# Optimization experiments

Measured on AMD Instinct MI355X. Metric: run time of the kernel, lower is better.

## Reference

```python
import jax, jax.numpy as jnp
import numpy as np

N = 131072   # total atoms in flat batch
E = 262144   # total bonds (directed edges)
G = 4096     # number of molecules (graphs)
FN = 30      # atom feature dim
FE = 11      # bond feature dim
H = 256      # hidden_dim
L = 5        # num GINE layers
BN_EPS = 1e-5


def _bn(x, g, b, m, v):
    # BatchNorm1d in eval mode: affine with running stats
    return g * (x - m) * jax.lax.rsqrt(v + BN_EPS) + b


def setup_inputs() -> dict:
    key = jax.random.key(0)
    ks = jax.random.split(key, 48)
    s = 0.05  # weight scale to keep 5-layer residual stack well-conditioned
    inp = {
        'x': jax.random.normal(ks[0], (N, FN), jnp.float32),
        'edge_index': jax.random.randint(ks[1], (2, E), 0, N),
        'batch': jnp.sort(jax.random.randint(ks[2], (N,), 0, G)),
        'edge_attr': jax.random.normal(ks[3], (E, FE), jnp.float32),
        # encoders
        'enc_w': s * jax.random.normal(ks[4], (FN, H), jnp.float32),
        'enc_b': jnp.zeros((H,), jnp.float32),
        'bond_w': s * jax.random.normal(ks[5], (FE, H), jnp.float32),
        'bond_b': jnp.zeros((H,), jnp.float32),
        # per-layer GINE params (stacked over L)
        'eps': jnp.zeros((L,), jnp.float32),
        'w1': s * jax.random.normal(ks[6], (L, H, 2 * H), jnp.float32),
        'b1': jnp.zeros((L, 2 * H), jnp.float32),
        'ibn_g': 1.0 + 0.1 * jax.random.normal(ks[7], (L, 2 * H), jnp.float32),
        'ibn_b': 0.1 * jax.random.normal(ks[8], (L, 2 * H), jnp.float32),
        'ibn_m': 0.1 * jax.random.normal(ks[9], (L, 2 * H), jnp.float32),
        'ibn_v': jnp.ones((L, 2 * H), jnp.float32),
        'w2': s * jax.random.normal(ks[10], (L, 2 * H, H), jnp.float32),
        'b2': jnp.zeros((L, H), jnp.float32),
        'obn_g': 1.0 + 0.1 * jax.random.normal(ks[11], (L, H), jnp.float32),
        'obn_b': 0.1 * jax.random.normal(ks[12], (L, H), jnp.float32),
        'obn_m': 0.1 * jax.random.normal(ks[13], (L, H), jnp.float32),
        'obn_v': jnp.ones((L, H), jnp.float32),
        # classifier
        'cw1': s * jax.random.normal(ks[14], (2 * H, H), jnp.float32),
        'cb1': jnp.zeros((H,), jnp.float32),
        'c1g': 1.0 + 0.1 * jax.random.normal(ks[15], (H,), jnp.float32),
        'c1b': 0.1 * jax.random.normal(ks[16], (H,), jnp.float32),
        'c1m': 0.1 * jax.random.normal(ks[17], (H,), jnp.float32),
        'c1v': jnp.ones((H,), jnp.float32),
        'cw2': s * jax.random.normal(ks[18], (H, H // 2), jnp.float32),
        'cb2': jnp.zeros((H // 2,), jnp.float32),
        'c2g': 1.0 + 0.1 * jax.random.normal(ks[19], (H // 2,), jnp.float32),
        'c2b': 0.1 * jax.random.normal(ks[20], (H // 2,), jnp.float32),
        'c2m': 0.1 * jax.random.normal(ks[21], (H // 2,), jnp.float32),
        'c2v': jnp.ones((H // 2,), jnp.float32),
        'cw3': s * jax.random.normal(ks[22], (H // 2, 1), jnp.float32),
        'cb3': jnp.zeros((1,), jnp.float32),
    }
    return inp


def reference(x, edge_index, batch, edge_attr,
              enc_w, enc_b, bond_w, bond_b,
              eps, w1, b1, ibn_g, ibn_b, ibn_m, ibn_v,
              w2, b2, obn_g, obn_b, obn_m, obn_v,
              cw1, cb1, c1g, c1b, c1m, c1v,
              cw2, cb2, c2g, c2b, c2m, c2v,
              cw3, cb3):
    n = x.shape[0]
    src, dst = edge_index[0], edge_index[1]
    h = x @ enc_w + enc_b                      # [N, H]
    e = edge_attr @ bond_w + bond_b           # [E, H]
    for i in range(L):
        h_in = h
        # GINEConv: (1+eps)*x_i + sum_j relu(x_j + e_ji), then MLP
        msg = jax.nn.relu(h[src] + e)                          # [E, H] gather
        agg = jax.ops.segment_sum(msg, dst, num_segments=n)    # [N, H] scatter-add
        z = (1.0 + eps[i]) * h + agg
        z = jax.nn.relu(_bn(z @ w1[i] + b1[i], ibn_g[i], ibn_b[i], ibn_m[i], ibn_v[i]))
        z = z @ w2[i] + b2[i]
        # outer BN + relu (dropout is identity in eval) + residual
        h = jax.nn.relu(_bn(z, obn_g[i], obn_b[i], obn_m[i], obn_v[i])) + h_in
    # global mean + max pooling by graph id
    counts = jax.ops.segment_sum(jnp.ones((n,), h.dtype), batch, num_segments=G)
    sums = jax.ops.segment_sum(h, batch, num_segments=G)
    mean_p = sums / jnp.maximum(counts, 1.0)[:, None]
    max_p = jax.ops.segment_max(h, batch, num_segments=G)
    max_p = jnp.where(counts[:, None] > 0, max_p, 0.0)
    p = jnp.concatenate([mean_p, max_p], axis=1)               # [G, 2H]
    # classifier (eval mode: dropout off, BN uses running stats)
    q = jax.nn.relu(_bn(p @ cw1 + cb1, c1g, c1b, c1m, c1v))
    q = jax.nn.relu(_bn(q @ cw2 + cb2, c2g, c2b, c2m, c2v))
    out = q @ cw3 + cb3
    return out[:, 0]                                           # [G]
```

## Files before the change

kernel.cpp:

```cpp
#include <hip/hip_runtime.h>
#include <math.h>

#define NA 131072
#define NE 262144
#define NG 4096
#define FN 30
#define FE 11
#define H  256
#define H2 512
#define NL 5
#define BN_EPS 1e-5f
#define KP 32

typedef _Float16 f16x8 __attribute__((ext_vector_type(8)));
typedef _Float16 f16x4 __attribute__((ext_vector_type(4)));
typedef float f32x4 __attribute__((ext_vector_type(4)));

#define GLOAD16(GP, LP) \
    __builtin_amdgcn_global_load_lds((const __attribute__((address_space(1))) void*)(GP), \
                                     (__attribute__((address_space(3))) void*)(LP), 16, 0, 0)

static char* g_buf = nullptr;
__attribute__((constructor)) static void _alloc_private_ws() {
    void* p = nullptr;
    if (hipMalloc(&p, (size_t)320 * 1024 * 1024) == hipSuccess) g_buf = (char*)p;
}

__global__ __launch_bounds__(256) void prep_w_all(const float* __restrict__ w, int K, int N,
                                                  _Float16* __restrict__ hT) {
    const float* wl = w + (size_t)blockIdx.z * K * N;
    _Float16* hTl = hT + (size_t)blockIdx.z * K * N;
    __shared__ float t[32][33];
    const int k0 = blockIdx.x * 32, n0 = blockIdx.y * 32;
    const int tx = threadIdx.x & 31, ty = threadIdx.x >> 5;
    #pragma unroll
    for (int i = 0; i < 4; ++i)
        t[ty + i * 8][tx] = wl[(size_t)(k0 + ty + i * 8) * N + n0 + tx];
    __syncthreads();
    #pragma unroll
    for (int i = 0; i < 4; ++i)
        hTl[(size_t)(n0 + ty + i * 8) * K + k0 + tx] = (_Float16)t[tx][ty + i * 8];
}

__global__ __launch_bounds__(256) void prep_w1s(const float* __restrict__ w1,
                                                _Float16* __restrict__ o) {
    const float* wl = w1 + (size_t)blockIdx.z * H * H2;
    _Float16* ol = o + (size_t)blockIdx.z * H * H2;
    const int c = blockIdx.x * 256 + threadIdx.x;
    const int slot = c & 3, row = (c >> 2) & 255, hk = c >> 10;
    const int n = (hk >> 3) * 256 + row;
    const int kb = (hk & 7) * 32 + (slot ^ ((row >> 1) & 3)) * 8;
    f16x8 v;
    #pragma unroll
    for (int e = 0; e < 8; ++e) v[e] = (_Float16)wl[(size_t)(kb + e) * H2 + n];
    *(f16x8*)(ol + (size_t)c * 8) = v;
}

__global__ __launch_bounds__(256) void prep_w2s(const float* __restrict__ w2,
                                                _Float16* __restrict__ o) {
    const float* wl = w2 + (size_t)blockIdx.z * H2 * H;
    _Float16* ol = o + (size_t)blockIdx.z * H2 * H;
    const int c = blockIdx.x * 256 + threadIdx.x;
    const int slot = c & 3, row = (c >> 2) & 255, ks = c >> 10;
    const int kb = ks * 32 + (slot ^ ((row >> 1) & 3)) * 8;
    f16x8 v;
    #pragma unroll
    for (int e = 0; e < 8; ++e) v[e] = (_Float16)wl[(size_t)(kb + e) * H + row];
    *(f16x8*)(ol + (size_t)c * 8) = v;
}

__global__ __launch_bounds__(256) void prep_wpad(const float* __restrict__ w, int K_IN,
                                                 _Float16* __restrict__ wT) {
    const int n = threadIdx.x;
    #pragma unroll
    for (int kk = 0; kk < KP / 8; ++kk) {
        f16x8 v;
        #pragma unroll
        for (int j = 0; j < 8; ++j) {
            const int k = kk * 8 + j;
            v[j] = (k < K_IN) ? (_Float16)w[(size_t)k * H + n] : (_Float16)0.0f;
        }
        *(f16x8*)(wT + (size_t)n * KP + kk * 8) = v;
    }
}

__global__ __launch_bounds__(256) void prep_x16(const float* __restrict__ x,
                                                _Float16* __restrict__ x16) {
    const int row = blockIdx.x * 64 + (threadIdx.x >> 2);
    const int g = threadIdx.x & 3;
    f16x8 v;
    #pragma unroll
    for (int j = 0; j < 8; ++j) {
        const int c = g * 8 + j;
        v[j] = (c < FN) ? (_Float16)x[(size_t)row * FN + c] : (_Float16)0.0f;
    }
    *(f16x8*)(x16 + (size_t)row * KP + g * 8) = v;
}

__global__ __launch_bounds__(256) void prep_ea16(const float* __restrict__ eattr,
                                                 const int2* __restrict__ se,
                                                 _Float16* __restrict__ ea16) {
    const int t = blockIdx.x * 64 + (threadIdx.x >> 2);
    const int g = threadIdx.x & 3;
    const int e = se[t].y;
    f16x8 v;
    #pragma unroll
    for (int j = 0; j < 8; ++j) {
        const int c = g * 8 + j;
        v[j] = (c < FE) ? (_Float16)eattr[(size_t)e * FE + c] : (_Float16)0.0f;
    }
    *(f16x8*)(ea16 + (size_t)t * KP + g * 8) = v;
}

__global__ __launch_bounds__(256) void count_deg(const int* __restrict__ ei,
                                                 int* __restrict__ deg) {
    const int e = blockIdx.x * 256 + threadIdx.x;
    if (e < NE) atomicAdd(&deg[ei[NE + e]], 1);
}

__global__ __launch_bounds__(1024) void scan_deg(const int* __restrict__ deg,
                                                 int* __restrict__ rowptr,
                                                 int* __restrict__ cursor) {
    __shared__ int part[1024];
    const int t = threadIdx.x;
    const int base = t * 128;
    int s = 0;
    #pragma unroll 8
    for (int i = 0; i < 128; ++i) s += deg[base + i];
    part[t] = s;
    __syncthreads();
    for (int off = 1; off < 1024; off <<= 1) {
        const int v = (t >= off) ? part[t - off] : 0;
        __syncthreads();
        part[t] += v;
        __syncthreads();
    }
    int run = (t == 0) ? 0 : part[t - 1];
    #pragma unroll 8
    for (int i = 0; i < 128; ++i) {
        rowptr[base + i] = run;
        cursor[base + i] = run;
        run += deg[base + i];
    }
    if (t == 1023) rowptr[NA] = run;
}

__global__ __launch_bounds__(256) void fill_elist(const int* __restrict__ ei,
                                                  int* __restrict__ cursor,
                                                  int2* __restrict__ se) {
    const int e = blockIdx.x * 256 + threadIdx.x;
    if (e < NE) {
        const int src = ei[e];
        const int pos = atomicAdd(&cursor[ei[NE + e]], 1);
        se[pos] = make_int2(src, e);
    }
}

__global__ __launch_bounds__(256) void gine_msg(const _Float16* __restrict__ h16,
                                                const _Float16* __restrict__ eb,
                                                const int2* __restrict__ se,
                                                const int* __restrict__ rowptr,
                                                const float* __restrict__ eps, int l,
                                                _Float16* __restrict__ z) {
    const int dst = blockIdx.x * 4 + (threadIdx.x >> 6);
    const int lane = threadIdx.x & 63;
    const int c = lane * 4;
    const float sc = 1.0f + eps[l];
    const f16x4 hv = *(const f16x4*)(h16 + (size_t)dst * H + c);
    float4 acc;
    acc.x = sc * (float)hv.x; acc.y = sc * (float)hv.y;
    acc.z = sc * (float)hv.z; acc.w = sc * (float)hv.w;
    const int lo = rowptr[dst], hi = rowptr[dst + 1];
    for (int t = lo; t < hi; ++t) {
        const int src = se[t].x;
        const f16x4 hs = *(const f16x4*)(h16 + (size_t)src * H + c);
        const f16x4 ev = *(const f16x4*)(eb + (size_t)t * H + c);
        acc.x += fmaxf((float)hs.x + (float)ev.x, 0.0f);
        acc.y += fmaxf((float)hs.y + (float)ev.y, 0.0f);
        acc.z += fmaxf((float)hs.z + (float)ev.z, 0.0f);
        acc.w += fmaxf((float)hs.w + (float)ev.w, 0.0f);
    }
    f16x4 o;
    o.x = (_Float16)acc.x; o.y = (_Float16)acc.y;
    o.z = (_Float16)acc.z; o.w = (_Float16)acc.w;
    *(f16x4*)(z + (size_t)dst * H + c) = o;
}

__global__ __launch_bounds__(512, 2) void fused_mlp(
    const _Float16* __restrict__ Az,
    const _Float16* __restrict__ W1S,
    const _Float16* __restrict__ W2S,
    const float* __restrict__ b1l, const float* __restrict__ ig,
    const float* __restrict__ ib, const float* __restrict__ im,
    const float* __restrict__ iv,
    const float* __restrict__ b2l, const float* __restrict__ og,
    const float* __restrict__ ob, const float* __restrict__ om,
    const float* __restrict__ ov,
    _Float16* __restrict__ Hio)
{
    __shared__ __align__(16) f16x8 Bs[2][1024];
    __shared__ _Float16 Z1[64 * 512];

    const int tid = threadIdx.x;
    const int m0 = blockIdx.x * 64;
    const int lane = tid & 63, wv = tid >> 6;
    const int lrow = lane & 15, lgrp = lane >> 4;
    const int wm2 = wv >> 2, wn2 = wv & 3;

    const int ar0 = m0 + wm2 * 32 + lrow;
    const int ar1 = ar0 + 16;

    #define STAGE(WS, TILE, CUR) { \
        const _Float16* gp_ = (WS) + ((size_t)(TILE) * 1024 + wv * 128) * 8 + (size_t)lane * 8; \
        char* lp_ = (char*)&Bs[0][0] + (CUR) * 16384 + wv * 2048; \
        GLOAD16(gp_, lp_); \
        GLOAD16(gp_ + 64 * 8, lp_ + 1024); }

    f16x8 afA0[8], afA1[8];
    #pragma unroll
    for (int ks = 0; ks < 8; ++ks) {
        afA0[ks] = *(const f16x8*)(Az + (size_t)ar0 * 256 + ks * 32 + lgrp * 8);
        afA1[ks] = *(const f16x8*)(Az + (size_t)ar1 * 256 + ks * 32 + lgrp * 8);
    }
    #pragma unroll
    for (int ks = 0; ks < 8; ++ks)
        asm volatile("" : "+v"(afA0[ks]), "+v"(afA1[ks]));

    const f32x4 zero4 = {0.0f, 0.0f, 0.0f, 0.0f};

    #pragma unroll 1
    for (int h = 0; h < 2; ++h) {
        float scl1[4], shf1[4];
        #pragma unroll
        for (int ni = 0; ni < 4; ++ni) {
            const int c = h * 256 + wn2 * 64 + ni * 16 + lrow;
            const float s = ig[c] * rsqrtf(iv[c] + BN_EPS);
            scl1[ni] = s;
            shf1[ni] = s * (b1l[c] - im[c]) + ib[c];
        }
        f32x4 acc[2][4];
        #pragma unroll
        for (int i = 0; i < 2; ++i)
            #pragma unroll
            for (int j = 0; j < 4; ++j) acc[i][j] = zero4;

        STAGE(W1S, h * 8, 0);
        __syncthreads();
        #pragma unroll
        for (int ks = 0; ks < 8; ++ks) {
            if (ks < 7) STAGE(W1S, h * 8 + ks + 1, (ks + 1) & 1);
            const f16x8* bp = &Bs[ks & 1][0];
            f16x8 bf[4];
            #pragma unroll
            for (int ni = 0; ni < 4; ++ni) {
                const int br = wn2 * 64 + ni * 16 + lrow;
                bf[ni] = bp[br * 4 + (lgrp ^ ((br >> 1) & 3))];
            }
            #pragma unroll
            for (int ni = 0; ni < 4; ++ni) {
                acc[0][ni] = __builtin_amdgcn_mfma_f32_16x16x32_f16(afA0[ks], bf[ni], acc[0][ni], 0, 0, 0);
                acc[1][ni] = __builtin_amdgcn_mfma_f32_16x16x32_f16(afA1[ks], bf[ni], acc[1][ni], 0, 0, 0);
            }
            __syncthreads();
        }
        #pragma unroll
        for (int mi = 0; mi < 2; ++mi)
            #pragma unroll
            for (int j = 0; j < 4; ++j) {
                const int row = wm2 * 32 + mi * 16 + lgrp * 4 + j;
                #pragma unroll
                for (int ni = 0; ni < 4; ++ni) {
                    const int col = h * 256 + wn2 * 64 + ni * 16 + lrow;
                    const int slot = (col >> 3) ^ (row & 7);
                    Z1[row * 512 + (slot << 3) + (col & 7)] =
                        (_Float16)fmaxf(scl1[ni] * acc[mi][ni][j] + shf1[ni], 0.0f);
                }
            }
    }

    float scl2[4], shf2[4];
    #pragma unroll
    for (int ni = 0; ni < 4; ++ni) {
        const int c = wn2 * 64 + ni * 16 + lrow;
        const float s = og[c] * rsqrtf(ov[c] + BN_EPS);
        scl2[ni] = s;
        shf2[ni] = s * (b2l[c] - om[c]) + ob[c];
    }
    f32x4 acc2[2][4];
    #pragma unroll
    for (int i = 0; i < 2; ++i)
        #pragma unroll
        for (int j = 0; j < 4; ++j) acc2[i][j] = zero4;

    STAGE(W2S, 0, 0);
    __syncthreads();
    #pragma unroll 1
    for (int ks = 0; ks < 16; ++ks) {
        if (ks < 15) STAGE(W2S, ks + 1, (ks + 1) & 1);
        const int k0 = ks * 32;
        const f16x8* bp = &Bs[ks & 1][0];
        f16x8 af[2], bf[4];
        #pragma unroll
        for (int mi = 0; mi < 2; ++mi) {
            const int ar = wm2 * 32 + mi * 16 + lrow;
            const int slot = ((k0 >> 3) + lgrp) ^ (ar & 7);
            af[mi] = *(const f16x8*)&Z1[ar * 512 + (slot << 3)];
        }
        #pragma unroll
        for (int ni = 0; ni < 4; ++ni) {
            const int br = wn2 * 64 + ni * 16 + lrow;
            bf[ni] = bp[br * 4 + (lgrp ^ ((br >> 1) & 3))];
        }
        #pragma unroll
        for (int mi = 0; mi < 2; ++mi)
            #pragma unroll
            for (int ni = 0; ni < 4; ++ni)
                acc2[mi][ni] = __builtin_amdgcn_mfma_f32_16x16x32_f16(af[mi], bf[ni], acc2[mi][ni], 0, 0, 0);
        __syncthreads();
    }
    #undef STAGE

    #pragma unroll
    for (int mi = 0; mi < 2; ++mi)
        #pragma unroll
        for (int j = 0; j < 4; ++j) {
            const int row = m0 + wm2 * 32 + mi * 16 + lgrp * 4 + j;
            #pragma unroll
            for (int ni = 0; ni < 4; ++ni) {
                const int col = wn2 * 64 + ni * 16 + lrow;
                float v = fmaxf(scl2[ni] * acc2[mi][ni][j] + shf2[ni], 0.0f);
                v += (float)Hio[(size_t)row * H + col];
                Hio[(size_t)row * H + col] = (_Float16)v;
            }
        }
}

template <int KDIM, int EPI>
__global__ __launch_bounds__(256, 4) void gemm_f16(
    const _Float16* __restrict__ A,
    const _Float16* __restrict__ BT,
    int Ncols,
    const float* __restrict__ bias, const float* __restrict__ bng,
    const float* __restrict__ bnb, const float* __restrict__ bnm,
    const float* __restrict__ bnv,
    _Float16* __restrict__ C16, const _Float16* __restrict__ res)
{
    __shared__ f16x8 As[2][512];
    __shared__ f16x8 Bs[2][512];

    const int tid = threadIdx.x;
    const int nt = Ncols >> 7;
    const int nwg = gridDim.x, orig = blockIdx.x;
    const int q = nwg >> 3, r = nwg & 7;
    const int xcd = orig & 7, rk = orig >> 3;
    const int wg = (xcd < r ? xcd * (q + 1) : r * (q + 1) + (xcd - r) * q) + rk;
    const int m0 = (wg / nt) * 128;
    const int n0 = (wg % nt) * 128;

    const int wid = tid >> 6, lane = tid & 63;
    const int wm = wid >> 1, wn = wid & 1;
    const int lrow = lane & 15, lgrp = lane >> 4;
    const int r0s = tid >> 2;
    const int kq  = tid & 3;
    const int sw0 = kq ^ ((r0s >> 1) & 3);
    const int sw1 = kq ^ (((r0s + 64) >> 1) & 3);

    f32x4 acc[4][4];
    const f32x4 zero4 = {0.0f, 0.0f, 0.0f, 0.0f};
    #pragma unroll
    for (int i = 0; i < 4; ++i)
        #pragma unroll
        for (int j = 0; j < 4; ++j) acc[i][j] = zero4;

    f16x8 a0, a1, b0, b1;
    #define SLOAD(K0)                                                             \
        a0 = *(const f16x8*)(A  + (size_t)(m0 + r0s) * KDIM + (K0) + kq * 8);     \
        a1 = *(const f16x8*)(A  + (size_t)(m0 + r0s + 64) * KDIM + (K0) + kq * 8);\
        b0 = *(const f16x8*)(BT + (size_t)(n0 + r0s) * KDIM + (K0) + kq * 8);     \
        b1 = *(const f16x8*)(BT + (size_t)(n0 + r0s + 64) * KDIM + (K0) + kq * 8);
    #define SWRITE(CUR)                                                           \
        As[CUR][r0s * 4 + sw0] = a0;  As[CUR][(r0s + 64) * 4 + sw1] = a1;         \
        Bs[CUR][r0s * 4 + sw0] = b0;  Bs[CUR][(r0s + 64) * 4 + sw1] = b1;

    SLOAD(0);
    int cur = 0;
    for (int k0 = 0; k0 < KDIM; k0 += 32) {
        SWRITE(cur);
        __syncthreads();
        if (k0 + 32 < KDIM) { SLOAD(k0 + 32); }
        f16x8 af[4], bf[4];
        #pragma unroll
        for (int mi = 0; mi < 4; ++mi) {
            const int ar = wm * 64 + mi * 16 + lrow;
            af[mi] = As[cur][ar * 4 + (lgrp ^ ((ar >> 1) & 3))];
        }
        #pragma unroll
        for (int ni = 0; ni < 4; ++ni) {
            const int br = wn * 64 + ni * 16 + lrow;
            bf[ni] = Bs[cur][br * 4 + (lgrp ^ ((br >> 1) & 3))];
        }
        #pragma unroll
        for (int mi = 0; mi < 4; ++mi)
            #pragma unroll
            for (int ni = 0; ni < 4; ++ni)
                acc[mi][ni] = __builtin_amdgcn_mfma_f32_16x16x32_f16(af[mi], bf[ni], acc[mi][ni], 0, 0, 0);
        cur ^= 1;
    }
    #undef SLOAD
    #undef SWRITE

    float scl[4], shf[4];
    #pragma unroll
    for (int ni = 0; ni < 4; ++ni) {
        const int c = n0 + wn * 64 + ni * 16 + lrow;
        if (EPI == 2) {
            scl[ni] = 1.0f;
            shf[ni] = bias[c];
        } else {
            const float s = bng[c] * rsqrtf(bnv[c] + BN_EPS);
            scl[ni] = s;
            shf[ni] = s * (bias[c] - bnm[c]) + bnb[c];
        }
    }
    #pragma unroll
    for (int mi = 0; mi < 4; ++mi)
        #pragma unroll
        for (int j = 0; j < 4; ++j) {
            const int row = m0 + wm * 64 + mi * 16 + lgrp * 4 + j;
            #pragma unroll
            for (int ni = 0; ni < 4; ++ni) {
                const int col = n0 + wn * 64 + ni * 16 + lrow;
                float v = scl[ni] * acc[mi][ni][j] + shf[ni];
                if (EPI != 2) v = fmaxf(v, 0.0f);
                C16[(size_t)row * Ncols + col] = (_Float16)v;
            }
        }
}

__global__ __launch_bounds__(H) void pool_kernel(const _Float16* __restrict__ h16,
                                                 const int* __restrict__ batch,
                                                 _Float16* __restrict__ p16) {
    const int g = blockIdx.x;
    const int c = threadIdx.x;
    int lo, hi;
    {
        int a = 0, b = NA;
        while (a < b) { int mid = (a + b) >> 1; if (batch[mid] < g) a = mid + 1; else b = mid; }
        lo = a;
        b = NA;
        while (a < b) { int mid = (a + b) >> 1; if (batch[mid] < g + 1) a = mid + 1; else b = mid; }
        hi = a;
    }
    float sum = 0.0f, mx = -INFINITY;
    for (int n = lo; n < hi; ++n) {
        const float v = (float)h16[(size_t)n * H + c];
        sum += v;
        mx = fmaxf(mx, v);
    }
    const int cnt = hi - lo;
    const float mean = (cnt > 0) ? sum / (float)cnt : 0.0f;
    if (cnt == 0) mx = 0.0f;
    p16[(size_t)g * H2 + c] = (_Float16)mean;
    p16[(size_t)g * H2 + H + c] = (_Float16)mx;
}

__global__ __launch_bounds__(64) void final_out(const _Float16* __restrict__ q2,
                                                const float* __restrict__ w,
                                                const float* __restrict__ b,
                                                float* __restrict__ out) {
    const int g = blockIdx.x;
    const int lane = threadIdx.x;
    float acc = (float)q2[(size_t)g * 128 + lane] * w[lane]
              + (float)q2[(size_t)g * 128 + 64 + lane] * w[64 + lane];
    #pragma unroll
    for (int off = 32; off > 0; off >>= 1) acc += __shfl_down(acc, off);
    if (lane == 0) out[g] = acc + b[0];
}

extern "C" void kernel_launch(void* const* d_in, const int* in_sizes, int n_in,
                              void* d_out, int out_size, void* d_ws, size_t ws_size,
                              hipStream_t stream) {
    const float* x      = (const float*)d_in[0];
    const int*   ei     = (const int*)d_in[1];
    const int*   batch  = (const int*)d_in[2];
    const float* eattr  = (const float*)d_in[3];
    const float* enc_w  = (const float*)d_in[4];
    const float* enc_b  = (const float*)d_in[5];
    const float* bond_w = (const float*)d_in[6];
    const float* bond_b = (const float*)d_in[7];
    const float* eps    = (const float*)d_in[8];
    const float* w1     = (const float*)d_in[9];
    const float* b1     = (const float*)d_in[10];
    const float* ibn_g  = (const float*)d_in[11];
    const float* ibn_b  = (const float*)d_in[12];
    const float* ibn_m  = (const float*)d_in[13];
    const float* ibn_v  = (const float*)d_in[14];
    const float* w2     = (const float*)d_in[15];
    const float* b2     = (const float*)d_in[16];
    const float* obn_g  = (const float*)d_in[17];
    const float* obn_b  = (const float*)d_in[18];
    const float* obn_m  = (const float*)d_in[19];
    const float* obn_v  = (const float*)d_in[20];
    const float* cw1    = (const float*)d_in[21];
    const float* cb1    = (const float*)d_in[22];
    const float* c1g    = (const float*)d_in[23];
    const float* c1b    = (const float*)d_in[24];
    const float* c1m    = (const float*)d_in[25];
    const float* c1v    = (const float*)d_in[26];
    const float* cw2    = (const float*)d_in[27];
    const float* cb2    = (const float*)d_in[28];
    const float* c2g    = (const float*)d_in[29];
    const float* c2b    = (const float*)d_in[30];
    const float* c2m    = (const float*)d_in[31];
    const float* c2v    = (const float*)d_in[32];
    const float* cw3    = (const float*)d_in[33];
    const float* cb3    = (const float*)d_in[34];
    float* out = (float*)d_out;

    const size_t WTE       = (size_t)NL * H * H2;
    const size_t CW1E      = (size_t)H2 * H;
    const size_t CW2E      = (size_t)H * (H / 2);
    const size_t EWE       = (size_t)H * KP;
    const size_t BWE       = (size_t)H * KP;
    const size_t wt_bytes  = (2 * WTE + CW1E + CW2E + EWE + BWE) * 2;
    const size_t csr_words = (size_t)3 * NA + 1 + 2 * (size_t)NE + 63;
    const size_t csr_bytes = csr_words * 4;
    const size_t eb_bytes  = (size_t)NE * H * 2;
    const size_t h16_bytes = (size_t)NA * H * 2;
    const size_t z_bytes   = (size_t)NA * H * 2;
    const size_t x16_bytes = (size_t)NA * KP * 2;
    const size_t ea_bytes  = (size_t)NE * KP * 2;
    const size_t need_full = wt_bytes + csr_bytes + eb_bytes + h16_bytes + z_bytes
                           + x16_bytes + ea_bytes;

    char* buf;
    if (ws_size >= need_full) { buf = (char*)d_ws; }
    else if (g_buf)           { buf = g_buf; }
    else                      { buf = (char*)d_ws; }

    _Float16* w1S  = (_Float16*)buf;
    _Float16* w2S  = w1S + WTE;
    _Float16* cw1T = w2S + WTE;
    _Float16* cw2T = cw1T + CW1E;
    _Float16* encT = cw2T + CW2E;
    _Float16* bndT = encT + EWE;
    int*  deg    = (int*)(buf + wt_bytes);
    int*  rowptr = deg + NA;
    int*  cursor = rowptr + NA + 1;
    int2* se     = (int2*)(cursor + NA);
    _Float16* eb  = (_Float16*)(buf + wt_bytes + csr_bytes);
    _Float16* h16 = (_Float16*)((char*)eb + eb_bytes);
    _Float16* z   = (_Float16*)((char*)h16 + h16_bytes);
    _Float16* x16  = (_Float16*)((char*)z + z_bytes);
    _Float16* ea16 = (_Float16*)((char*)x16 + x16_bytes);

    _Float16* p16 = z;
    _Float16* q1  = p16 + (size_t)NG * H2;
    _Float16* q2  = q1 + (size_t)NG * H;

    prep_w1s<<<dim3(64, 1, NL), 256, 0, stream>>>(w1, w1S);
    prep_w2s<<<dim3(64, 1, NL), 256, 0, stream>>>(w2, w2S);
    prep_w_all<<<dim3(H2 / 32, H / 32, 1), 256, 0, stream>>>(cw1, H2, H, cw1T);
    prep_w_all<<<dim3(H / 32, H / 64, 1), 256, 0, stream>>>(cw2, H, H / 2, cw2T);
    prep_wpad<<<1, 256, 0, stream>>>(enc_w, FN, encT);
    prep_wpad<<<1, 256, 0, stream>>>(bond_w, FE, bndT);

    hipMemsetAsync(deg, 0, (size_t)NA * 4, stream);
    count_deg<<<NE / 256, 256, 0, stream>>>(ei, deg);
    scan_deg<<<1, 1024, 0, stream>>>(deg, rowptr, cursor);
    fill_elist<<<NE / 256, 256, 0, stream>>>(ei, cursor, se);

    prep_x16<<<NA / 64, 256, 0, stream>>>(x, x16);
    prep_ea16<<<NE / 64, 256, 0, stream>>>(eattr, se, ea16);

    gemm_f16<KP, 2><<<(NA / 128) * (H / 128), 256, 0, stream>>>(
        x16, encT, H, enc_b, nullptr, nullptr, nullptr, nullptr, h16, nullptr);
    gemm_f16<KP, 2><<<(NE / 128) * (H / 128), 256, 0, stream>>>(
        ea16, bndT, H, bond_b, nullptr, nullptr, nullptr, nullptr, eb, nullptr);

    for (int l = 0; l < NL; ++l) {
        gine_msg<<<NA / 4, 256, 0, stream>>>(h16, eb, se, rowptr, eps, l, z);
        fused_mlp<<<NA / 64, 512, 0, stream>>>(
            z, w1S + (size_t)l * H * H2, w2S + (size_t)l * H2 * H,
            b1 + (size_t)l * H2, ibn_g + (size_t)l * H2, ibn_b + (size_t)l * H2,
            ibn_m + (size_t)l * H2, ibn_v + (size_t)l * H2,
            b2 + (size_t)l * H, obn_g + (size_t)l * H, obn_b + (size_t)l * H,
            obn_m + (size_t)l * H, obn_v + (size_t)l * H,
            h16);
    }

    pool_kernel<<<NG, H, 0, stream>>>(h16, batch, p16);
    gemm_f16<H2, 0><<<(NG / 128) * (H / 128), 256, 0, stream>>>(
        p16, cw1T, H, cb1, c1g, c1b, c1m, c1v, q1, nullptr);
    gemm_f16<H, 0><<<(NG / 128) * ((H / 2) / 128), 256, 0, stream>>>(
        q1, cw2T, H / 2, cb2, c2g, c2b, c2m, c2v, q2, nullptr);
    final_out<<<NG, 64, 0, stream>>>(q2, cw3, cb3, out);
}
```

Measured before the change: 1.409 ms.

## Triple-buffer weight tiles in fused MLP with one barrier per k-step

The fused MLP kernel now keeps three LDS buffers for weight tiles instead of two and prefetches two tiles ahead. Each k-step uses a single `s_waitcnt vmcnt(2)` plus barrier instead of a barrier after every step. The prefetch stream runs continuously from the W1 tiles into the first W2 tiles, so the second GEMM no longer starts with a cold load. The goal is to hide global-to-LDS latency and cut barrier stalls. The cost is 16KB more shared memory and fully unrolled loops, which raises code size and register pressure.

```diff
diff --git a/kernel.cpp b/kernel.cpp
--- a/kernel.cpp
+++ b/kernel.cpp
@@ -198,7 +198,7 @@
     const float* __restrict__ ov,
     _Float16* __restrict__ Hio)
 {
-    __shared__ __align__(16) f16x8 Bs[2][1024];
+    __shared__ __align__(16) f16x8 Bs[3][1024];
     __shared__ _Float16 Z1[64 * 512];
 
     const int tid = threadIdx.x;
@@ -216,6 +216,12 @@
         GLOAD16(gp_, lp_); \
         GLOAD16(gp_ + 64 * 8, lp_ + 1024); }
 
+    #define SYNC_STEP() { \
+        asm volatile("s_waitcnt vmcnt(2)" ::: "memory"); \
+        __builtin_amdgcn_sched_barrier(0); \
+        __builtin_amdgcn_s_barrier(); \
+        __builtin_amdgcn_sched_barrier(0); }
+
     f16x8 afA0[8], afA1[8];
     #pragma unroll
     for (int ks = 0; ks < 8; ++ks) {
@@ -226,9 +232,12 @@
     for (int ks = 0; ks < 8; ++ks)
         asm volatile("" : "+v"(afA0[ks]), "+v"(afA1[ks]));
 
+    STAGE(W1S, 0, 0);
+    STAGE(W1S, 1, 1);
+
     const f32x4 zero4 = {0.0f, 0.0f, 0.0f, 0.0f};
 
-    #pragma unroll 1
+    #pragma unroll
     for (int h = 0; h < 2; ++h) {
         float scl1[4], shf1[4];
         #pragma unroll
@@ -244,12 +253,14 @@
             #pragma unroll
             for (int j = 0; j < 4; ++j) acc[i][j] = zero4;
 
-        STAGE(W1S, h * 8, 0);
-        __syncthreads();
         #pragma unroll
         for (int ks = 0; ks < 8; ++ks) {
-            if (ks < 7) STAGE(W1S, h * 8 + ks + 1, (ks + 1) & 1);
-            const f16x8* bp = &Bs[ks & 1][0];
+            const int t = h * 8 + ks;
+            SYNC_STEP();
+            const int tt = t + 2;
+            if (tt < 16)      { STAGE(W1S, tt, tt % 3); }
+            else              { STAGE(W2S, tt - 16, tt % 3); }
+            const f16x8* bp = &Bs[t % 3][0];
             f16x8 bf[4];
             #pragma unroll
             for (int ni = 0; ni < 4; ++ni) {
@@ -261,7 +272,6 @@
                 acc[0][ni] = __builtin_amdgcn_mfma_f32_16x16x32_f16(afA0[ks], bf[ni], acc[0][ni], 0, 0, 0);
                 acc[1][ni] = __builtin_amdgcn_mfma_f32_16x16x32_f16(afA1[ks], bf[ni], acc[1][ni], 0, 0, 0);
             }
-            __syncthreads();
         }
         #pragma unroll
         for (int mi = 0; mi < 2; ++mi)
@@ -278,6 +288,8 @@
             }
     }
 
+    __syncthreads();
+
     float scl2[4], shf2[4];
     #pragma unroll
     for (int ni = 0; ni < 4; ++ni) {
@@ -292,13 +304,14 @@
         #pragma unroll
         for (int j = 0; j < 4; ++j) acc2[i][j] = zero4;
 
-    STAGE(W2S, 0, 0);
-    __syncthreads();
-    #pragma unroll 1
+    #pragma unroll
     for (int ks = 0; ks < 16; ++ks) {
-        if (ks < 15) STAGE(W2S, ks + 1, (ks + 1) & 1);
+        const int t = 16 + ks;
+        if (ks > 0) SYNC_STEP();
+        const int tt = t + 2;
+        if (tt < 32) { STAGE(W2S, tt - 16, tt % 3); }
         const int k0 = ks * 32;
-        const f16x8* bp = &Bs[ks & 1][0];
+        const f16x8* bp = &Bs[t % 3][0];
         f16x8 af[2], bf[4];
         #pragma unroll
         for (int mi = 0; mi < 2; ++mi) {
@@ -316,9 +329,9 @@
             #pragma unroll
             for (int ni = 0; ni < 4; ++ni)
                 acc2[mi][ni] = __builtin_amdgcn_mfma_f32_16x16x32_f16(af[mi], bf[ni], acc2[mi][ni], 0, 0, 0);
-        __syncthreads();
     }
     #undef STAGE
+    #undef SYNC_STEP
 
     #pragma unroll
     for (int mi = 0; mi < 2; ++mi)
```

Result: faster. 1.329 ms (-5.7%).
